# Optimization experiments

Hardware: AMD Instinct MI355X
Metric: run time of the kernel (lower is better)

The kernel has to match this reference:

```python
import jax, jax.numpy as jnp
import numpy as np

B, T, HW, ENC, DEC, ATT, EMB, V = 32, 128, 14, 2048, 512, 512, 512, 10000
P = HW * HW  # num_pixels = 196


def setup_inputs() -> dict:
    key = jax.random.key(0)
    ks = jax.random.split(key, 24)
    s = 0.02
    inp = {
        'bimgs': jax.random.normal(ks[0], (B, HW, HW, ENC), dtype=jnp.float32),
        'bx': jax.random.randint(ks[1], (B, T), 0, V),
        # torch code assumes lengths sorted DESCENDING
        'bxlen': jnp.sort(jax.random.randint(ks[2], (B,), 1, T + 1))[::-1],
        'emb_W': jax.random.normal(ks[3], (V, EMB)) * s,
        'enc_att_W': jax.random.normal(ks[4], (ATT, ENC)) * s,
        'enc_att_b': jnp.zeros((ATT,)),
        'dec_att_W': jax.random.normal(ks[5], (ATT, DEC)) * s,
        'dec_att_b': jnp.zeros((ATT,)),
        'full_att_W': jax.random.normal(ks[6], (1, ATT)) * s,
        'full_att_b': jnp.zeros((1,)),
        'init_h_W': jax.random.normal(ks[7], (DEC, ENC)) * s,
        'init_h_b': jnp.zeros((DEC,)),
        'init_c_W': jax.random.normal(ks[8], (DEC, ENC)) * s,
        'init_c_b': jnp.zeros((DEC,)),
        'f_beta_W': jax.random.normal(ks[9], (ENC, DEC)) * s,
        'f_beta_b': jnp.zeros((ENC,)),
        'W_ih': jax.random.normal(ks[10], (4 * DEC, EMB + ENC)) * s,
        'b_ih': jnp.zeros((4 * DEC,)),
        'W_hh': jax.random.normal(ks[11], (4 * DEC, DEC)) * s,
        'b_hh': jnp.zeros((4 * DEC,)),
        'fc_W': jax.random.normal(ks[12], (V, DEC)) * s,
        'fc_b': jnp.zeros((V,)),
    }
    return inp


def reference(bimgs, bx, bxlen, emb_W, enc_att_W, enc_att_b, dec_att_W, dec_att_b,
              full_att_W, full_att_b, init_h_W, init_h_b, init_c_W, init_c_b,
              f_beta_W, f_beta_b, W_ih, b_ih, W_hh, b_hh, fc_W, fc_b):
    b = bimgs.shape[0]
    imgs = bimgs.reshape(b, -1, bimgs.shape[-1])          # [B,P,enc]
    t_len = bx.shape[-1]
    embeds = emb_W[bx]                                     # [B,T,E]
    mean_img = imgs.mean(axis=1)                           # [B,enc]
    h0 = mean_img @ init_h_W.T + init_h_b                  # [B,dec]
    c0 = mean_img @ init_c_W.T + init_c_b
    # encoder attention projection is time-invariant -> hoist out of the loop
    att1 = imgs @ enc_att_W.T + enc_att_b                  # [B,P,A]
    active_ts = jnp.arange(t_len)[:, None] < bxlen[None, :]  # [T,B]
    emb_ts = embeds.transpose(1, 0, 2)                     # [T,B,E]

    def step(carry, xs):
        h, c = carry
        emb_t, active = xs
        att2 = h @ dec_att_W.T + dec_att_b                 # [B,A]
        e = jax.nn.relu(att1 + att2[:, None, :]) @ full_att_W[0] + full_att_b[0]  # [B,P]
        alpha = jax.nn.softmax(e, axis=1)
        awe = jnp.einsum('bpe,bp->be', imgs, alpha)        # [B,enc]
        gate = jax.nn.sigmoid(h @ f_beta_W.T + f_beta_b)
        x = jnp.concatenate([emb_t, gate * awe], axis=1)   # [B,E+enc]
        # PyTorch LSTMCell: gate order i, f, g, o
        gates = x @ W_ih.T + b_ih + h @ W_hh.T + b_hh
        i_, f_, g_, o_ = jnp.split(gates, 4, axis=1)
        i_ = jax.nn.sigmoid(i_); f_ = jax.nn.sigmoid(f_); o_ = jax.nn.sigmoid(o_)
        g_ = jnp.tanh(g_)
        c_new = f_ * c + i_ * g_
        h_new = o_ * jnp.tanh(c_new)
        preds = h_new @ fc_W.T + fc_b                      # dropout = identity (eval)
        m = active[:, None]
        h2 = jnp.where(m, h_new, h)
        c2 = jnp.where(m, c_new, c)
        return (h2, c2), (jnp.where(m, preds, 0.0), jnp.where(m, alpha, 0.0))

    _, (preds_ts, alphas_ts) = jax.lax.scan(step, (h0, c0), (emb_ts, active_ts))
    predictions = preds_ts.transpose(1, 0, 2)              # [B,T,V]
    alphas = alphas_ts.transpose(1, 0, 2)                  # [B,T,P]
    return predictions, alphas
```

## Files before the change

### kernel.cpp

```cpp
#include <hip/hip_runtime.h>
#include <hip/hip_bf16.h>

#define BB 32
#define TT 128
#define PP 196
#define ENC 2048
#define DEC 512
#define ATT 512
#define EMB 512
#define VV 10000
#define G4 2048
#define KX 2560

typedef unsigned short u16;
typedef unsigned int u32;
typedef __attribute__((ext_vector_type(8))) short short8;
typedef __attribute__((ext_vector_type(4))) float f32x4;

__device__ __forceinline__ float bf2f(u16 u) { return __uint_as_float(((u32)u) << 16); }
__device__ __forceinline__ u16 f2bf(float f) {
  u32 x = __float_as_uint(f);
  u32 r = (x + 0x7fffu + ((x >> 16) & 1u)) >> 16;
  return (u16)r;
}
__device__ __forceinline__ void unpack8(uint4 v, float* f) {
  f[0] = __uint_as_float(v.x << 16); f[1] = __uint_as_float(v.x & 0xffff0000u);
  f[2] = __uint_as_float(v.y << 16); f[3] = __uint_as_float(v.y & 0xffff0000u);
  f[4] = __uint_as_float(v.z << 16); f[5] = __uint_as_float(v.z & 0xffff0000u);
  f[6] = __uint_as_float(v.w << 16); f[7] = __uint_as_float(v.w & 0xffff0000u);
}
__device__ __forceinline__ void load8(const float* __restrict__ p, float* f) {
  float4 a = ((const float4*)p)[0];
  float4 b = ((const float4*)p)[1];
  f[0] = a.x; f[1] = a.y; f[2] = a.z; f[3] = a.w;
  f[4] = b.x; f[5] = b.y; f[6] = b.z; f[7] = b.w;
}
__device__ __forceinline__ float sigf(float x) { return 1.0f / (1.0f + __expf(-x)); }
__device__ __forceinline__ short8 ld_frag(const u16* __restrict__ p) {
  union { uint4 u; short8 s; } cv;
  cv.u = *(const uint4*)p;
  return cv.s;
}

__global__ __launch_bounds__(256) void k_cvt(const float* __restrict__ src, u16* __restrict__ dst, int n) {
  int i0 = (blockIdx.x * 256 + threadIdx.x) * 8;
  if (i0 >= n) return;
  float f[8]; load8(src + i0, f);
  u16 o[8];
#pragma unroll
  for (int u = 0; u < 8; u++) o[u] = f2bf(f[u]);
  *(uint4*)(dst + i0) = *(const uint4*)o;
}

__global__ __launch_bounds__(256) void k_mean(const u16* __restrict__ imgs_bf, u16* __restrict__ mean_bf) {
  int b = blockIdx.x >> 2, chunk = blockIdx.x & 3;
  int ch0 = chunk * 512 + threadIdx.x * 2;
  const u32* base = (const u32*)(imgs_bf + (size_t)b * PP * ENC + ch0);
  float a0 = 0.f, a1 = 0.f;
#pragma unroll 4
  for (int p = 0; p < PP; p++) {
    u32 u = base[(size_t)p * (ENC / 2)];
    a0 += __uint_as_float(u << 16);
    a1 += __uint_as_float(u & 0xffff0000u);
  }
  const float inv = 1.0f / PP;
  u16 o[2] = { f2bf(a0 * inv), f2bf(a1 * inv) };
  *(u32*)(mean_bf + b * ENC + ch0) = *(const u32*)o;
}

__global__ __launch_bounds__(64) void k_init2(const u16* __restrict__ W2_bf,
    const float* __restrict__ ihb, const float* __restrict__ icb,
    const u16* __restrict__ mean_bf, u16* __restrict__ h_bf, float* __restrict__ c) {
  int lane = threadIdx.x;
  int j0 = blockIdx.x * 16;
  int m = lane & 15, quad = lane >> 4;
  const u16* arow = W2_bf + (size_t)(j0 + m) * ENC + quad * 8;
  const u16* xb0 = mean_bf + (size_t)m * ENC + quad * 8;
  const u16* xb1 = mean_bf + (size_t)(16 + m) * ENC + quad * 8;
  f32x4 acc0 = {0.f,0.f,0.f,0.f}, acc1 = {0.f,0.f,0.f,0.f};
  for (int k = 0; k < ENC; k += 32) {
    short8 a = ld_frag(arow + k);
    short8 x0 = ld_frag(xb0 + k);
    short8 x1 = ld_frag(xb1 + k);
    acc0 = __builtin_amdgcn_mfma_f32_16x16x32_bf16(a, x0, acc0, 0, 0, 0);
    acc1 = __builtin_amdgcn_mfma_f32_16x16x32_bf16(a, x1, acc1, 0, 0, 0);
  }
  int jj = j0 + quad * 4;
  int b0 = m, b1 = 16 + m;
#pragma unroll
  for (int r = 0; r < 4; r++) {
    int j = jj + r;
    if (j < 512) {
      float bia = ihb[j];
      h_bf[b0 * DEC + j] = f2bf(acc0[r] + bia);
      h_bf[b1 * DEC + j] = f2bf(acc1[r] + bia);
    } else {
      int g = j - 512;
      float bia = icb[g];
      c[b0 * DEC + g] = acc0[r] + bia;
      c[b1 * DEC + g] = acc1[r] + bia;
    }
  }
}

__global__ __launch_bounds__(256) void k_att1(const u16* __restrict__ imgs_bf,
    const u16* __restrict__ encW_bf, const float* __restrict__ encb, u16* __restrict__ att1) {
  int tid = threadIdx.x;
  int wave = tid >> 6, lane = tid & 63;
  int m0 = blockIdx.x * 32;
  int lm = lane & 15, quad = lane >> 4;
  const u16* b0p = imgs_bf + (size_t)(m0 + lm) * ENC + quad * 8;
  const u16* b1p = imgs_bf + (size_t)(m0 + 16 + lm) * ENC + quad * 8;
  const u16* arow = encW_bf + (size_t)(wave * 128 + lm) * ENC + quad * 8;
  f32x4 acc[8][2];
#pragma unroll
  for (int i = 0; i < 8; i++) { acc[i][0] = (f32x4){0.f,0.f,0.f,0.f}; acc[i][1] = (f32x4){0.f,0.f,0.f,0.f}; }
  for (int k = 0; k < ENC; k += 32) {
    short8 B0 = ld_frag(b0p + k);
    short8 B1 = ld_frag(b1p + k);
#pragma unroll
    for (int i = 0; i < 8; i++) {
      short8 A = ld_frag(arow + (size_t)i * 16 * ENC + k);
      acc[i][0] = __builtin_amdgcn_mfma_f32_16x16x32_bf16(A, B0, acc[i][0], 0, 0, 0);
      acc[i][1] = __builtin_amdgcn_mfma_f32_16x16x32_bf16(A, B1, acc[i][1], 0, 0, 0);
    }
  }
#pragma unroll
  for (int i = 0; i < 8; i++) {
    int jb = wave * 128 + i * 16 + quad * 4;
#pragma unroll
    for (int r = 0; r < 4; r++) {
      int j = jb + r;
      float bia = encb[j];
      att1[(size_t)(m0 + lm) * ATT + j]      = f2bf(acc[i][0][r] + bia);
      att1[(size_t)(m0 + 16 + lm) * ATT + j] = f2bf(acc[i][1][r] + bia);
    }
  }
}

__global__ __launch_bounds__(64) void k_stage1(int t,
    const int* __restrict__ bx, const int* __restrict__ bxlen,
    const u16* __restrict__ W3, const float* __restrict__ decb,
    const float* __restrict__ fbb, const float* __restrict__ bhh,
    const u16* __restrict__ h_bf,
    float* __restrict__ att2, float* __restrict__ gate, float* __restrict__ hWhh,
    const u16* __restrict__ fcW_bf, const float* __restrict__ fcb, float* __restrict__ preds,
    const float* __restrict__ embW, u16* __restrict__ x_bf) {
  int bid = blockIdx.x;
  int lane = threadIdx.x;
  if (bid < 288) {
    if (t >= TT) return;
    int j0 = bid * 16;
    int m = lane & 15, quad = lane >> 4;
    const u16* arow = W3 + (size_t)(j0 + m) * DEC + quad * 8;
    const u16* xb0 = h_bf + (size_t)m * DEC + quad * 8;
    const u16* xb1 = h_bf + (size_t)(16 + m) * DEC + quad * 8;
    f32x4 acc0 = {0.f,0.f,0.f,0.f}, acc1 = {0.f,0.f,0.f,0.f};
    for (int k = 0; k < DEC; k += 32) {
      short8 a = ld_frag(arow + k);
      short8 x0 = ld_frag(xb0 + k);
      short8 x1 = ld_frag(xb1 + k);
      acc0 = __builtin_amdgcn_mfma_f32_16x16x32_bf16(a, x0, acc0, 0, 0, 0);
      acc1 = __builtin_amdgcn_mfma_f32_16x16x32_bf16(a, x1, acc1, 0, 0, 0);
    }
    int jj = j0 + quad * 4;
    int b0 = m, b1 = 16 + m;
#pragma unroll
    for (int r = 0; r < 4; r++) {
      int j = jj + r;
      float v0 = acc0[r], v1 = acc1[r];
      if (j0 < ATT) {
        float bia = decb[j];
        att2[b0 * ATT + j] = v0 + bia;
        att2[b1 * ATT + j] = v1 + bia;
      } else if (j0 < ATT + ENC) {
        int g = j - ATT;
        float bia = fbb[g];
        gate[b0 * ENC + g] = sigf(v0 + bia);
        gate[b1 * ENC + g] = sigf(v1 + bia);
      } else {
        int g = j - ATT - ENC;
        float bia = bhh[g];
        hWhh[b0 * G4 + g] = v0 + bia;
        hWhh[b1 * G4 + g] = v1 + bia;
      }
    }
  } else if (bid < 913) {
    if (t == 0) return;
    int tfc = t - 1;
    int j0 = (bid - 288) * 16;
    int m = lane & 15, quad = lane >> 4;
    const u16* arow = fcW_bf + (size_t)(j0 + m) * DEC + quad * 8;
    const u16* xb0 = h_bf + (size_t)m * DEC + quad * 8;
    const u16* xb1 = h_bf + (size_t)(16 + m) * DEC + quad * 8;
    f32x4 acc0 = {0.f,0.f,0.f,0.f}, acc1 = {0.f,0.f,0.f,0.f};
    for (int k = 0; k < DEC; k += 32) {
      short8 a = ld_frag(arow + k);
      short8 x0 = ld_frag(xb0 + k);
      short8 x1 = ld_frag(xb1 + k);
      acc0 = __builtin_amdgcn_mfma_f32_16x16x32_bf16(a, x0, acc0, 0, 0, 0);
      acc1 = __builtin_amdgcn_mfma_f32_16x16x32_bf16(a, x1, acc1, 0, 0, 0);
    }
    int jj = j0 + quad * 4;
    int b0 = m, b1 = 16 + m;
    bool act0 = (tfc < bxlen[b0]);
    bool act1 = (tfc < bxlen[b1]);
#pragma unroll
    for (int r = 0; r < 4; r++) {
      int j = jj + r;
      float bia = fcb[j];
      preds[((size_t)b0 * TT + tfc) * VV + j] = act0 ? (acc0[r] + bia) : 0.f;
      preds[((size_t)b1 * TT + tfc) * VV + j] = act1 ? (acc1[r] + bia) : 0.f;
    }
  } else {
    if (t >= TT) return;
    int flat = (bid - 913) * 64 + lane;
    int b = flat >> 5;
    int ch0 = (flat & 31) * 16;
    int tok = bx[b * TT + t];
    const float* e = embW + (size_t)tok * EMB + ch0;
    u16 o[16];
#pragma unroll
    for (int u = 0; u < 16; u++) o[u] = f2bf(e[u]);
    *(uint4*)(x_bf + (size_t)b * KX + ch0)     = *(const uint4*)o;
    *(uint4*)(x_bf + (size_t)b * KX + ch0 + 8) = *(const uint4*)(o + 8);
  }
}

__global__ __launch_bounds__(256) void k_att(int t, const int* __restrict__ bxlen,
    const u16* __restrict__ att1, const float* __restrict__ att2,
    const float* __restrict__ faW, const float* __restrict__ fab,
    float* __restrict__ alpha_ws, float* __restrict__ out_alphas) {
  int b = blockIdx.x;
  int tid = threadIdx.x;
  if (t >= bxlen[b]) {
    if (tid < PP) out_alphas[((size_t)b * TT + t) * PP + tid] = 0.f;
    return;
  }
  __shared__ float a2[ATT];
  __shared__ float w_s[ATT];
  __shared__ float redw[4], redw2[4];
  for (int i = tid; i < ATT; i += 256) { a2[i] = att2[b * ATT + i]; w_s[i] = faW[i]; }
  __syncthreads();
  float e = -1e30f;
  if (tid < PP) {
    const uint4* ar = (const uint4*)(att1 + (size_t)(b * PP + tid) * ATT);
    float acc = 0.f;
    for (int k = 0; k < ATT; k += 8) {
      float af[8]; unpack8(ar[k >> 3], af);
#pragma unroll
      for (int u = 0; u < 8; u++) {
        float v = af[u] + a2[k + u];
        acc += fmaxf(v, 0.f) * w_s[k + u];
      }
    }
    e = acc + fab[0];
  }
  int lane = tid & 63, wid = tid >> 6;
  float wmax = e;
#pragma unroll
  for (int off = 32; off; off >>= 1) wmax = fmaxf(wmax, __shfl_xor(wmax, off));
  if (lane == 0) redw[wid] = wmax;
  __syncthreads();
  float mx = fmaxf(fmaxf(redw[0], redw[1]), fmaxf(redw[2], redw[3]));
  float ex = (tid < PP) ? __expf(e - mx) : 0.f;
  float wsum = ex;
#pragma unroll
  for (int off = 32; off; off >>= 1) wsum += __shfl_xor(wsum, off);
  if (lane == 0) redw2[wid] = wsum;
  __syncthreads();
  float inv = 1.0f / (redw2[0] + redw2[1] + redw2[2] + redw2[3]);
  if (tid < PP) {
    float al = ex * inv;
    alpha_ws[b * PP + tid] = al;
    out_alphas[((size_t)b * TT + t) * PP + tid] = al;
  }
}

__global__ __launch_bounds__(256) void k_awe(int t, const int* __restrict__ bxlen,
    const u16* __restrict__ imgs_bf, const float* __restrict__ alpha_ws,
    const float* __restrict__ gate, u16* __restrict__ x_bf) {
  int b = blockIdx.x >> 2, chunk = blockIdx.x & 3;
  if (t >= bxlen[b]) return;
  __shared__ float al[PP];
  int tid = threadIdx.x;
  if (tid < PP) al[tid] = alpha_ws[b * PP + tid];
  __syncthreads();
  int ch0 = chunk * 512 + tid * 2;
  const u32* base = (const u32*)(imgs_bf + (size_t)b * PP * ENC + ch0);
  float acc0 = 0.f, acc1 = 0.f;
#pragma unroll 4
  for (int p = 0; p < PP; p++) {
    u32 u = base[(size_t)p * (ENC / 2)];
    float a = al[p];
    acc0 += a * __uint_as_float(u << 16);
    acc1 += a * __uint_as_float(u & 0xffff0000u);
  }
  float2 g = *(const float2*)(gate + b * ENC + ch0);
  u16 o[2] = { f2bf(g.x * acc0), f2bf(g.y * acc1) };
  *(u32*)(x_bf + (size_t)b * KX + EMB + ch0) = *(const u32*)o;
}

__global__ __launch_bounds__(64) void k_gates(const u16* __restrict__ Wih_bf,
    const u16* __restrict__ x_bf, float* __restrict__ gates_p) {
  int lane = threadIdx.x;
  int j0 = blockIdx.x * 16;
  int kc = blockIdx.y * 640;
  int m = lane & 15, quad = lane >> 4;
  const u16* arow = Wih_bf + (size_t)(j0 + m) * KX + kc + quad * 8;
  const u16* xb0 = x_bf + (size_t)m * KX + kc + quad * 8;
  const u16* xb1 = x_bf + (size_t)(16 + m) * KX + kc + quad * 8;
  f32x4 acc0 = {0.f,0.f,0.f,0.f}, acc1 = {0.f,0.f,0.f,0.f};
  for (int k = 0; k < 640; k += 32) {
    short8 a = ld_frag(arow + k);
    short8 x0 = ld_frag(xb0 + k);
    short8 x1 = ld_frag(xb1 + k);
    acc0 = __builtin_amdgcn_mfma_f32_16x16x32_bf16(a, x0, acc0, 0, 0, 0);
    acc1 = __builtin_amdgcn_mfma_f32_16x16x32_bf16(a, x1, acc1, 0, 0, 0);
  }
  float* gp = gates_p + (size_t)blockIdx.y * BB * G4;
  int jj = j0 + quad * 4;
  int b0 = m, b1 = 16 + m;
#pragma unroll
  for (int r = 0; r < 4; r++) {
    int j = jj + r;
    gp[b0 * G4 + j] = acc0[r];
    gp[b1 * G4 + j] = acc1[r];
  }
}

__global__ __launch_bounds__(256) void k_lstm(int t, const int* __restrict__ bxlen,
    const float* __restrict__ gates_p, const float* __restrict__ bih,
    const float* __restrict__ hWhh,
    u16* __restrict__ h_bf, float* __restrict__ c) {
  int idx = blockIdx.x * 256 + threadIdx.x;
  int b = idx >> 9, d = idx & 511;
  if (t >= bxlen[b]) return;
  float pre[4];
#pragma unroll
  for (int g = 0; g < 4; g++) {
    int j = g * 512 + d;
    float s = bih[j] + hWhh[b * G4 + j];
#pragma unroll
    for (int cc = 0; cc < 4; cc++) s += gates_p[(size_t)cc * BB * G4 + b * G4 + j];
    pre[g] = s;
  }
  float i_ = sigf(pre[0]);
  float f_ = sigf(pre[1]);
  float g_ = tanhf(pre[2]);
  float o_ = sigf(pre[3]);
  float cn = f_ * c[b * DEC + d] + i_ * g_;
  float hn = o_ * tanhf(cn);
  c[b * DEC + d] = cn;
  h_bf[b * DEC + d] = f2bf(hn);
}

extern "C" void kernel_launch(void* const* d_in, const int* in_sizes, int n_in,
                              void* d_out, int out_size, void* d_ws, size_t ws_size,
                              hipStream_t stream) {
  const float* imgs = (const float*)d_in[0];
  const int* bx     = (const int*)d_in[1];
  const int* bxlen  = (const int*)d_in[2];
  const float* embW = (const float*)d_in[3];
  const float* encW = (const float*)d_in[4];
  const float* encb = (const float*)d_in[5];
  const float* decW = (const float*)d_in[6];
  const float* decb = (const float*)d_in[7];
  const float* faW  = (const float*)d_in[8];
  const float* fab  = (const float*)d_in[9];
  const float* ihW  = (const float*)d_in[10];
  const float* ihb  = (const float*)d_in[11];
  const float* icW  = (const float*)d_in[12];
  const float* icb  = (const float*)d_in[13];
  const float* fbW  = (const float*)d_in[14];
  const float* fbb  = (const float*)d_in[15];
  const float* Wih  = (const float*)d_in[16];
  const float* bih  = (const float*)d_in[17];
  const float* Whh  = (const float*)d_in[18];
  const float* bhh  = (const float*)d_in[19];
  const float* fcW  = (const float*)d_in[20];
  const float* fcb  = (const float*)d_in[21];

  float* out_preds  = (float*)d_out;
  float* out_alphas = out_preds + (size_t)BB * TT * VV;

  char* wsb = (char*)d_ws;
  size_t off = 0;
  u16* imgs_bf = (u16*)(wsb + off); off += (size_t)BB * PP * ENC * 2;
  u16* W3_bf   = (u16*)(wsb + off); off += (size_t)4608 * DEC * 2;
  u16* Wih_bf  = (u16*)(wsb + off); off += (size_t)G4 * KX * 2;
  u16* fcW_bf  = (u16*)(wsb + off); off += (size_t)VV * DEC * 2;
  u16* encW_bf = (u16*)(wsb + off); off += (size_t)ATT * ENC * 2;
  u16* att1    = (u16*)(wsb + off);
  u16* W2_bf   = att1;
  u16* mean_bf = att1 + (size_t)1024 * ENC;
  off += (size_t)BB * PP * ATT * 2;
  u16* x_bf    = (u16*)(wsb + off); off += (size_t)BB * KX * 2;
  u16* h_bf    = (u16*)(wsb + off); off += (size_t)BB * DEC * 2;
  float* c      = (float*)(wsb + off); off += (size_t)BB * DEC * 4;
  float* att2   = (float*)(wsb + off); off += (size_t)BB * ATT * 4;
  float* gate   = (float*)(wsb + off); off += (size_t)BB * ENC * 4;
  float* hWhh   = (float*)(wsb + off); off += (size_t)BB * G4 * 4;
  float* gates_p = (float*)(wsb + off); off += (size_t)4 * BB * G4 * 4;
  float* alpha  = (float*)(wsb + off); off += (size_t)BB * PP * 4;

  k_cvt<<<(BB * PP * ENC) / 2048, 256, 0, stream>>>(imgs, imgs_bf, BB * PP * ENC);
  k_cvt<<<(DEC * DEC) / 2048, 256, 0, stream>>>(decW, W3_bf, DEC * DEC);
  k_cvt<<<(ENC * DEC) / 2048, 256, 0, stream>>>(fbW, W3_bf + (size_t)DEC * DEC, ENC * DEC);
  k_cvt<<<(G4 * DEC) / 2048, 256, 0, stream>>>(Whh, W3_bf + (size_t)(DEC + ENC) * DEC, G4 * DEC);
  k_cvt<<<(G4 * KX) / 2048, 256, 0, stream>>>(Wih, Wih_bf, G4 * KX);
  k_cvt<<<(VV * DEC) / 2048, 256, 0, stream>>>(fcW, fcW_bf, VV * DEC);
  k_cvt<<<(ATT * ENC) / 2048, 256, 0, stream>>>(encW, encW_bf, ATT * ENC);
  k_cvt<<<(DEC * ENC) / 2048, 256, 0, stream>>>(ihW, W2_bf, DEC * ENC);
  k_cvt<<<(DEC * ENC) / 2048, 256, 0, stream>>>(icW, W2_bf + (size_t)DEC * ENC, DEC * ENC);

  k_mean<<<BB * 4, 256, 0, stream>>>(imgs_bf, mean_bf);
  k_init2<<<64, 64, 0, stream>>>(W2_bf, ihb, icb, mean_bf, h_bf, c);
  k_att1<<<(BB * PP) / 32, 256, 0, stream>>>(imgs_bf, encW_bf, encb, att1);

  for (int t = 0; t < TT; t++) {
    k_stage1<<<929, 64, 0, stream>>>(t, bx, bxlen, W3_bf, decb, fbb, bhh, h_bf,
                                     att2, gate, hWhh, fcW_bf, fcb, out_preds, embW, x_bf);
    k_att<<<BB, 256, 0, stream>>>(t, bxlen, att1, att2, faW, fab, alpha, out_alphas);
    k_awe<<<BB * 4, 256, 0, stream>>>(t, bxlen, imgs_bf, alpha, gate, x_bf);
    k_gates<<<dim3(G4 / 16, 4), 64, 0, stream>>>(Wih_bf, x_bf, gates_p);
    k_lstm<<<(BB * DEC) / 256, 256, 0, stream>>>(t, bxlen, gates_p, bih, hWhh, h_bf, c);
  }
  k_stage1<<<929, 64, 0, stream>>>(TT, bx, bxlen, W3_bf, decb, fbb, bhh, h_bf,
                                   att2, gate, hWhh, fcW_bf, fcb, out_preds, embW, x_bf);
}
```

Measured before the change: 6.786 ms.

## Fuse attention with weighted encoding and gate GEMM with LSTM cell

Merges the attention-score/softmax kernel with the attention-weighted-encoding kernel in a single 1024-thread block per batch row, keeping alpha in shared memory. It also merges the input-gate GEMM with the LSTM cell update: each block computes all four gate slices for 16 hidden units over the full K dimension, then applies the cell update from shared memory. This cuts per-step launches from five to three and removes the global round trips for alpha and the split-K partial gates. The cost is less parallelism: the gate GEMM drops from 512 split-K waves to 128 waves, each running the full K loop serially.

New measurement: 9.066 ms. 33.6% more time.

```diff
diff --git a/kernel.cpp b/kernel.cpp
--- a/kernel.cpp
+++ b/kernel.cpp
@@ -227,10 +227,11 @@
   }
 }
 
-__global__ __launch_bounds__(256) void k_att(int t, const int* __restrict__ bxlen,
+__global__ __launch_bounds__(1024) void k_attawe(int t, const int* __restrict__ bxlen,
     const u16* __restrict__ att1, const float* __restrict__ att2,
     const float* __restrict__ faW, const float* __restrict__ fab,
-    float* __restrict__ alpha_ws, float* __restrict__ out_alphas) {
+    const u16* __restrict__ imgs_bf, const float* __restrict__ gate,
+    float* __restrict__ out_alphas, u16* __restrict__ x_bf) {
   int b = blockIdx.x;
   int tid = threadIdx.x;
   if (t >= bxlen[b]) {
@@ -239,60 +240,58 @@
   }
   __shared__ float a2[ATT];
   __shared__ float w_s[ATT];
-  __shared__ float redw[4], redw2[4];
-  for (int i = tid; i < ATT; i += 256) { a2[i] = att2[b * ATT + i]; w_s[i] = faW[i]; }
-  __syncthreads();
-  float e = -1e30f;
-  if (tid < PP) {
-    const uint4* ar = (const uint4*)(att1 + (size_t)(b * PP + tid) * ATT);
+  __shared__ float alph[PP];
+  __shared__ float red1[16], red2[16];
+  if (tid < ATT) a2[tid] = att2[b * ATT + tid];
+  else w_s[tid - ATT] = faW[tid - ATT];
+  __syncthreads();
+  int p = tid >> 2, sub = tid & 3;
+  if (p < PP) {
+    const uint4* ar = (const uint4*)(att1 + (size_t)(b * PP + p) * ATT + sub * 128);
+    int kb = sub * 128;
     float acc = 0.f;
-    for (int k = 0; k < ATT; k += 8) {
+#pragma unroll
+    for (int k = 0; k < 128; k += 8) {
       float af[8]; unpack8(ar[k >> 3], af);
 #pragma unroll
       for (int u = 0; u < 8; u++) {
-        float v = af[u] + a2[k + u];
-        acc += fmaxf(v, 0.f) * w_s[k + u];
+        float v = af[u] + a2[kb + k + u];
+        acc += fmaxf(v, 0.f) * w_s[kb + k + u];
       }
     }
-    e = acc + fab[0];
-  }
+    acc += __shfl_xor(acc, 1);
+    acc += __shfl_xor(acc, 2);
+    if (sub == 0) alph[p] = acc + fab[0];
+  }
+  __syncthreads();
+  float v = (tid < PP) ? alph[tid] : -1e30f;
   int lane = tid & 63, wid = tid >> 6;
-  float wmax = e;
+  float wmax = v;
 #pragma unroll
   for (int off = 32; off; off >>= 1) wmax = fmaxf(wmax, __shfl_xor(wmax, off));
-  if (lane == 0) redw[wid] = wmax;
-  __syncthreads();
-  float mx = fmaxf(fmaxf(redw[0], redw[1]), fmaxf(redw[2], redw[3]));
-  float ex = (tid < PP) ? __expf(e - mx) : 0.f;
+  if (lane == 0) red1[wid] = wmax;
+  __syncthreads();
+  float mx = fmaxf(fmaxf(red1[0], red1[1]), fmaxf(red1[2], red1[3]));
+  float ex = (tid < PP) ? __expf(v - mx) : 0.f;
   float wsum = ex;
 #pragma unroll
   for (int off = 32; off; off >>= 1) wsum += __shfl_xor(wsum, off);
-  if (lane == 0) redw2[wid] = wsum;
-  __syncthreads();
-  float inv = 1.0f / (redw2[0] + redw2[1] + redw2[2] + redw2[3]);
+  if (lane == 0) red2[wid] = wsum;
+  __syncthreads();
+  float inv = 1.0f / (red2[0] + red2[1] + red2[2] + red2[3]);
   if (tid < PP) {
     float al = ex * inv;
-    alpha_ws[b * PP + tid] = al;
+    alph[tid] = al;
     out_alphas[((size_t)b * TT + t) * PP + tid] = al;
   }
-}
-
-__global__ __launch_bounds__(256) void k_awe(int t, const int* __restrict__ bxlen,
-    const u16* __restrict__ imgs_bf, const float* __restrict__ alpha_ws,
-    const float* __restrict__ gate, u16* __restrict__ x_bf) {
-  int b = blockIdx.x >> 2, chunk = blockIdx.x & 3;
-  if (t >= bxlen[b]) return;
-  __shared__ float al[PP];
-  int tid = threadIdx.x;
-  if (tid < PP) al[tid] = alpha_ws[b * PP + tid];
-  __syncthreads();
-  int ch0 = chunk * 512 + tid * 2;
+  __syncthreads();
+  int ch0 = tid * 2;
   const u32* base = (const u32*)(imgs_bf + (size_t)b * PP * ENC + ch0);
   float acc0 = 0.f, acc1 = 0.f;
 #pragma unroll 4
-  for (int p = 0; p < PP; p++) {
-    u32 u = base[(size_t)p * (ENC / 2)];
-    float a = al[p];
+  for (int pp = 0; pp < PP; pp++) {
+    u32 u = base[(size_t)pp * (ENC / 2)];
+    float a = alph[pp];
     acc0 += a * __uint_as_float(u << 16);
     acc1 += a * __uint_as_float(u & 0xffff0000u);
   }
@@ -301,58 +300,49 @@
   *(u32*)(x_bf + (size_t)b * KX + EMB + ch0) = *(const u32*)o;
 }
 
-__global__ __launch_bounds__(64) void k_gates(const u16* __restrict__ Wih_bf,
-    const u16* __restrict__ x_bf, float* __restrict__ gates_p) {
-  int lane = threadIdx.x;
-  int j0 = blockIdx.x * 16;
-  int kc = blockIdx.y * 640;
+__global__ __launch_bounds__(256) void k_gateslstm(int t, const int* __restrict__ bxlen,
+    const u16* __restrict__ Wih_bf, const float* __restrict__ bih,
+    const u16* __restrict__ x_bf, const float* __restrict__ hWhh,
+    u16* __restrict__ h_bf, float* __restrict__ c) {
+  __shared__ float pre_s[4][16][33];
+  int tid = threadIdx.x;
+  int wave = tid >> 6, lane = tid & 63;
+  int g = blockIdx.x;
   int m = lane & 15, quad = lane >> 4;
-  const u16* arow = Wih_bf + (size_t)(j0 + m) * KX + kc + quad * 8;
-  const u16* xb0 = x_bf + (size_t)m * KX + kc + quad * 8;
-  const u16* xb1 = x_bf + (size_t)(16 + m) * KX + kc + quad * 8;
+  int jbase = wave * 512 + g * 16;
+  const u16* arow = Wih_bf + (size_t)(jbase + m) * KX + quad * 8;
+  const u16* xb0 = x_bf + (size_t)m * KX + quad * 8;
+  const u16* xb1 = x_bf + (size_t)(16 + m) * KX + quad * 8;
   f32x4 acc0 = {0.f,0.f,0.f,0.f}, acc1 = {0.f,0.f,0.f,0.f};
-  for (int k = 0; k < 640; k += 32) {
+#pragma unroll 4
+  for (int k = 0; k < KX; k += 32) {
     short8 a = ld_frag(arow + k);
     short8 x0 = ld_frag(xb0 + k);
     short8 x1 = ld_frag(xb1 + k);
     acc0 = __builtin_amdgcn_mfma_f32_16x16x32_bf16(a, x0, acc0, 0, 0, 0);
     acc1 = __builtin_amdgcn_mfma_f32_16x16x32_bf16(a, x1, acc1, 0, 0, 0);
   }
-  float* gp = gates_p + (size_t)blockIdx.y * BB * G4;
-  int jj = j0 + quad * 4;
-  int b0 = m, b1 = 16 + m;
+  int dd = quad * 4;
 #pragma unroll
   for (int r = 0; r < 4; r++) {
-    int j = jj + r;
-    gp[b0 * G4 + j] = acc0[r];
-    gp[b1 * G4 + j] = acc1[r];
-  }
-}
-
-__global__ __launch_bounds__(256) void k_lstm(int t, const int* __restrict__ bxlen,
-    const float* __restrict__ gates_p, const float* __restrict__ bih,
-    const float* __restrict__ hWhh,
-    u16* __restrict__ h_bf, float* __restrict__ c) {
-  int idx = blockIdx.x * 256 + threadIdx.x;
-  int b = idx >> 9, d = idx & 511;
-  if (t >= bxlen[b]) return;
-  float pre[4];
-#pragma unroll
-  for (int g = 0; g < 4; g++) {
-    int j = g * 512 + d;
-    float s = bih[j] + hWhh[b * G4 + j];
-#pragma unroll
-    for (int cc = 0; cc < 4; cc++) s += gates_p[(size_t)cc * BB * G4 + b * G4 + j];
-    pre[g] = s;
-  }
-  float i_ = sigf(pre[0]);
-  float f_ = sigf(pre[1]);
-  float g_ = tanhf(pre[2]);
-  float o_ = sigf(pre[3]);
-  float cn = f_ * c[b * DEC + d] + i_ * g_;
-  float hn = o_ * tanhf(cn);
-  c[b * DEC + d] = cn;
-  h_bf[b * DEC + d] = f2bf(hn);
+    pre_s[wave][dd + r][m]      = acc0[r];
+    pre_s[wave][dd + r][16 + m] = acc1[r];
+  }
+  __syncthreads();
+  for (int i = tid; i < 512; i += 256) {
+    int d_idx = i >> 5, b = i & 31;
+    if (t >= bxlen[b]) continue;
+    int d = g * 16 + d_idx;
+    float p0 = pre_s[0][d_idx][b] + bih[d]        + hWhh[b * G4 + d];
+    float p1 = pre_s[1][d_idx][b] + bih[512 + d]  + hWhh[b * G4 + 512 + d];
+    float p2 = pre_s[2][d_idx][b] + bih[1024 + d] + hWhh[b * G4 + 1024 + d];
+    float p3 = pre_s[3][d_idx][b] + bih[1536 + d] + hWhh[b * G4 + 1536 + d];
+    float i_ = sigf(p0), f_ = sigf(p1), g_ = tanhf(p2), o_ = sigf(p3);
+    float cn = f_ * c[b * DEC + d] + i_ * g_;
+    float hn = o_ * tanhf(cn);
+    c[b * DEC + d] = cn;
+    h_bf[b * DEC + d] = f2bf(hn);
+  }
 }
 
 extern "C" void kernel_launch(void* const* d_in, const int* in_sizes, int n_in,
@@ -401,8 +391,6 @@
   float* att2   = (float*)(wsb + off); off += (size_t)BB * ATT * 4;
   float* gate   = (float*)(wsb + off); off += (size_t)BB * ENC * 4;
   float* hWhh   = (float*)(wsb + off); off += (size_t)BB * G4 * 4;
-  float* gates_p = (float*)(wsb + off); off += (size_t)4 * BB * G4 * 4;
-  float* alpha  = (float*)(wsb + off); off += (size_t)BB * PP * 4;
 
   k_cvt<<<(BB * PP * ENC) / 2048, 256, 0, stream>>>(imgs, imgs_bf, BB * PP * ENC);
   k_cvt<<<(DEC * DEC) / 2048, 256, 0, stream>>>(decW, W3_bf, DEC * DEC);
@@ -421,10 +409,9 @@
   for (int t = 0; t < TT; t++) {
     k_stage1<<<929, 64, 0, stream>>>(t, bx, bxlen, W3_bf, decb, fbb, bhh, h_bf,
                                      att2, gate, hWhh, fcW_bf, fcb, out_preds, embW, x_bf);
-    k_att<<<BB, 256, 0, stream>>>(t, bxlen, att1, att2, faW, fab, alpha, out_alphas);
-    k_awe<<<BB * 4, 256, 0, stream>>>(t, bxlen, imgs_bf, alpha, gate, x_bf);
-    k_gates<<<dim3(G4 / 16, 4), 64, 0, stream>>>(Wih_bf, x_bf, gates_p);
-    k_lstm<<<(BB * DEC) / 256, 256, 0, stream>>>(t, bxlen, gates_p, bih, hWhh, h_bf, c);
+    k_attawe<<<BB, 1024, 0, stream>>>(t, bxlen, att1, att2, faW, fab, imgs_bf, gate,
+                                      out_alphas, x_bf);
+    k_gateslstm<<<BB, 256, 0, stream>>>(t, bxlen, Wih_bf, bih, x_bf, hWhh, h_bf, c);
   }
   k_stage1<<<929, 64, 0, stream>>>(TT, bx, bxlen, W3_bf, decb, fbb, bhh, h_bf,
                                    att2, gate, hWhh, fcW_bf, fcb, out_preds, embW, x_bf);
```

## Hoist output projection out of recurrence into one batched GEMM over all steps

Applied to the files above, without the earlier changes.

The vocabulary projection no longer runs inside every time step. Each step's hidden state is now stored in a history buffer, and after the loop one large MFMA GEMM computes all predictions with a weight tile shared across 32 rows. Embedding lookups for every step are also gathered and converted to bf16 once up front, and the input-gate GEMM is split into five K-chunks to match the separate embedding and attention-context buffers. This removes re-streaming the 10k×512 fc weight on each step and shortens the serial per-step chain, at the cost of extra workspace and one more partial-sum read in the LSTM kernel.

Measured after the change: 6.265 ms. 1.08x faster.

```diff
diff --git a/kernel.cpp b/kernel.cpp
--- a/kernel.cpp
+++ b/kernel.cpp
@@ -9,6 +9,7 @@
 #define ATT 512
 #define EMB 512
 #define VV 10000
+#define VVP 10240
 #define G4 2048
 #define KX 2560
 
@@ -50,6 +51,20 @@
 #pragma unroll
   for (int u = 0; u < 8; u++) o[u] = f2bf(f[u]);
   *(uint4*)(dst + i0) = *(const uint4*)o;
+}
+
+__global__ __launch_bounds__(256) void k_emball(const int* __restrict__ bx,
+    const float* __restrict__ embW, u16* __restrict__ xemb) {
+  int flat = blockIdx.x * 256 + threadIdx.x;
+  int row = flat >> 6;
+  int c8 = (flat & 63) * 8;
+  int tok = bx[row];
+  const float* e = embW + (size_t)tok * EMB + c8;
+  float f[8]; load8(e, f);
+  u16 o[8];
+#pragma unroll
+  for (int u = 0; u < 8; u++) o[u] = f2bf(f[u]);
+  *(uint4*)(xemb + (size_t)row * EMB + c8) = *(const uint4*)o;
 }
 
 __global__ __launch_bounds__(256) void k_mean(const u16* __restrict__ imgs_bf, u16* __restrict__ mean_bf) {
@@ -138,92 +153,45 @@
   }
 }
 
-__global__ __launch_bounds__(64) void k_stage1(int t,
-    const int* __restrict__ bx, const int* __restrict__ bxlen,
-    const u16* __restrict__ W3, const float* __restrict__ decb,
-    const float* __restrict__ fbb, const float* __restrict__ bhh,
+__global__ __launch_bounds__(64) void k_step1(const u16* __restrict__ W3,
+    const float* __restrict__ decb, const float* __restrict__ fbb, const float* __restrict__ bhh,
     const u16* __restrict__ h_bf,
-    float* __restrict__ att2, float* __restrict__ gate, float* __restrict__ hWhh,
-    const u16* __restrict__ fcW_bf, const float* __restrict__ fcb, float* __restrict__ preds,
-    const float* __restrict__ embW, u16* __restrict__ x_bf) {
-  int bid = blockIdx.x;
+    float* __restrict__ att2, float* __restrict__ gate, float* __restrict__ hWhh) {
   int lane = threadIdx.x;
-  if (bid < 288) {
-    if (t >= TT) return;
-    int j0 = bid * 16;
-    int m = lane & 15, quad = lane >> 4;
-    const u16* arow = W3 + (size_t)(j0 + m) * DEC + quad * 8;
-    const u16* xb0 = h_bf + (size_t)m * DEC + quad * 8;
-    const u16* xb1 = h_bf + (size_t)(16 + m) * DEC + quad * 8;
-    f32x4 acc0 = {0.f,0.f,0.f,0.f}, acc1 = {0.f,0.f,0.f,0.f};
-    for (int k = 0; k < DEC; k += 32) {
-      short8 a = ld_frag(arow + k);
-      short8 x0 = ld_frag(xb0 + k);
-      short8 x1 = ld_frag(xb1 + k);
-      acc0 = __builtin_amdgcn_mfma_f32_16x16x32_bf16(a, x0, acc0, 0, 0, 0);
-      acc1 = __builtin_amdgcn_mfma_f32_16x16x32_bf16(a, x1, acc1, 0, 0, 0);
-    }
-    int jj = j0 + quad * 4;
-    int b0 = m, b1 = 16 + m;
-#pragma unroll
-    for (int r = 0; r < 4; r++) {
-      int j = jj + r;
-      float v0 = acc0[r], v1 = acc1[r];
-      if (j0 < ATT) {
-        float bia = decb[j];
-        att2[b0 * ATT + j] = v0 + bia;
-        att2[b1 * ATT + j] = v1 + bia;
-      } else if (j0 < ATT + ENC) {
-        int g = j - ATT;
-        float bia = fbb[g];
-        gate[b0 * ENC + g] = sigf(v0 + bia);
-        gate[b1 * ENC + g] = sigf(v1 + bia);
-      } else {
-        int g = j - ATT - ENC;
-        float bia = bhh[g];
-        hWhh[b0 * G4 + g] = v0 + bia;
-        hWhh[b1 * G4 + g] = v1 + bia;
-      }
-    }
-  } else if (bid < 913) {
-    if (t == 0) return;
-    int tfc = t - 1;
-    int j0 = (bid - 288) * 16;
-    int m = lane & 15, quad = lane >> 4;
-    const u16* arow = fcW_bf + (size_t)(j0 + m) * DEC + quad * 8;
-    const u16* xb0 = h_bf + (size_t)m * DEC + quad * 8;
-    const u16* xb1 = h_bf + (size_t)(16 + m) * DEC + quad * 8;
-    f32x4 acc0 = {0.f,0.f,0.f,0.f}, acc1 = {0.f,0.f,0.f,0.f};
-    for (int k = 0; k < DEC; k += 32) {
-      short8 a = ld_frag(arow + k);
-      short8 x0 = ld_frag(xb0 + k);
-      short8 x1 = ld_frag(xb1 + k);
-      acc0 = __builtin_amdgcn_mfma_f32_16x16x32_bf16(a, x0, acc0, 0, 0, 0);
-      acc1 = __builtin_amdgcn_mfma_f32_16x16x32_bf16(a, x1, acc1, 0, 0, 0);
-    }
-    int jj = j0 + quad * 4;
-    int b0 = m, b1 = 16 + m;
-    bool act0 = (tfc < bxlen[b0]);
-    bool act1 = (tfc < bxlen[b1]);
-#pragma unroll
-    for (int r = 0; r < 4; r++) {
-      int j = jj + r;
-      float bia = fcb[j];
-      preds[((size_t)b0 * TT + tfc) * VV + j] = act0 ? (acc0[r] + bia) : 0.f;
-      preds[((size_t)b1 * TT + tfc) * VV + j] = act1 ? (acc1[r] + bia) : 0.f;
-    }
-  } else {
-    if (t >= TT) return;
-    int flat = (bid - 913) * 64 + lane;
-    int b = flat >> 5;
-    int ch0 = (flat & 31) * 16;
-    int tok = bx[b * TT + t];
-    const float* e = embW + (size_t)tok * EMB + ch0;
-    u16 o[16];
-#pragma unroll
-    for (int u = 0; u < 16; u++) o[u] = f2bf(e[u]);
-    *(uint4*)(x_bf + (size_t)b * KX + ch0)     = *(const uint4*)o;
-    *(uint4*)(x_bf + (size_t)b * KX + ch0 + 8) = *(const uint4*)(o + 8);
+  int j0 = blockIdx.x * 16;
+  int m = lane & 15, quad = lane >> 4;
+  const u16* arow = W3 + (size_t)(j0 + m) * DEC + quad * 8;
+  const u16* xb0 = h_bf + (size_t)m * DEC + quad * 8;
+  const u16* xb1 = h_bf + (size_t)(16 + m) * DEC + quad * 8;
+  f32x4 acc0 = {0.f,0.f,0.f,0.f}, acc1 = {0.f,0.f,0.f,0.f};
+  for (int k = 0; k < DEC; k += 32) {
+    short8 a = ld_frag(arow + k);
+    short8 x0 = ld_frag(xb0 + k);
+    short8 x1 = ld_frag(xb1 + k);
+    acc0 = __builtin_amdgcn_mfma_f32_16x16x32_bf16(a, x0, acc0, 0, 0, 0);
+    acc1 = __builtin_amdgcn_mfma_f32_16x16x32_bf16(a, x1, acc1, 0, 0, 0);
+  }
+  int jj = j0 + quad * 4;
+  int b0 = m, b1 = 16 + m;
+#pragma unroll
+  for (int r = 0; r < 4; r++) {
+    int j = jj + r;
+    float v0 = acc0[r], v1 = acc1[r];
+    if (j0 < ATT) {
+      float bia = decb[j];
+      att2[b0 * ATT + j] = v0 + bia;
+      att2[b1 * ATT + j] = v1 + bia;
+    } else if (j0 < ATT + ENC) {
+      int g = j - ATT;
+      float bia = fbb[g];
+      gate[b0 * ENC + g] = sigf(v0 + bia);
+      gate[b1 * ENC + g] = sigf(v1 + bia);
+    } else {
+      int g = j - ATT - ENC;
+      float bia = bhh[g];
+      hWhh[b0 * G4 + g] = v0 + bia;
+      hWhh[b1 * G4 + g] = v1 + bia;
+    }
   }
 }
 
@@ -279,7 +247,7 @@
 
 __global__ __launch_bounds__(256) void k_awe(int t, const int* __restrict__ bxlen,
     const u16* __restrict__ imgs_bf, const float* __restrict__ alpha_ws,
-    const float* __restrict__ gate, u16* __restrict__ x_bf) {
+    const float* __restrict__ gate, u16* __restrict__ x_awe) {
   int b = blockIdx.x >> 2, chunk = blockIdx.x & 3;
   if (t >= bxlen[b]) return;
   __shared__ float al[PP];
@@ -298,27 +266,36 @@
   }
   float2 g = *(const float2*)(gate + b * ENC + ch0);
   u16 o[2] = { f2bf(g.x * acc0), f2bf(g.y * acc1) };
-  *(u32*)(x_bf + (size_t)b * KX + EMB + ch0) = *(const u32*)o;
-}
-
-__global__ __launch_bounds__(64) void k_gates(const u16* __restrict__ Wih_bf,
-    const u16* __restrict__ x_bf, float* __restrict__ gates_p) {
+  *(u32*)(x_awe + (size_t)b * ENC + ch0) = *(const u32*)o;
+}
+
+__global__ __launch_bounds__(64) void k_gates(int t, const u16* __restrict__ Wih_bf,
+    const u16* __restrict__ xemb, const u16* __restrict__ x_awe,
+    float* __restrict__ gates_p) {
   int lane = threadIdx.x;
   int j0 = blockIdx.x * 16;
-  int kc = blockIdx.y * 640;
+  int y = blockIdx.y;
+  int kofs = y * 512;
   int m = lane & 15, quad = lane >> 4;
-  const u16* arow = Wih_bf + (size_t)(j0 + m) * KX + kc + quad * 8;
-  const u16* xb0 = x_bf + (size_t)m * KX + kc + quad * 8;
-  const u16* xb1 = x_bf + (size_t)(16 + m) * KX + kc + quad * 8;
+  const u16* arow = Wih_bf + (size_t)(j0 + m) * KX + kofs + quad * 8;
+  const u16 *b0p, *b1p;
+  if (y == 0) {
+    b0p = xemb + ((size_t)m * TT + t) * EMB + quad * 8;
+    b1p = xemb + ((size_t)(16 + m) * TT + t) * EMB + quad * 8;
+  } else {
+    int ao = kofs - 512;
+    b0p = x_awe + (size_t)m * ENC + ao + quad * 8;
+    b1p = x_awe + (size_t)(16 + m) * ENC + ao + quad * 8;
+  }
   f32x4 acc0 = {0.f,0.f,0.f,0.f}, acc1 = {0.f,0.f,0.f,0.f};
-  for (int k = 0; k < 640; k += 32) {
+  for (int k = 0; k < 512; k += 32) {
     short8 a = ld_frag(arow + k);
-    short8 x0 = ld_frag(xb0 + k);
-    short8 x1 = ld_frag(xb1 + k);
+    short8 x0 = ld_frag(b0p + k);
+    short8 x1 = ld_frag(b1p + k);
     acc0 = __builtin_amdgcn_mfma_f32_16x16x32_bf16(a, x0, acc0, 0, 0, 0);
     acc1 = __builtin_amdgcn_mfma_f32_16x16x32_bf16(a, x1, acc1, 0, 0, 0);
   }
-  float* gp = gates_p + (size_t)blockIdx.y * BB * G4;
+  float* gp = gates_p + (size_t)y * BB * G4;
   int jj = j0 + quad * 4;
   int b0 = m, b1 = 16 + m;
 #pragma unroll
@@ -332,7 +309,7 @@
 __global__ __launch_bounds__(256) void k_lstm(int t, const int* __restrict__ bxlen,
     const float* __restrict__ gates_p, const float* __restrict__ bih,
     const float* __restrict__ hWhh,
-    u16* __restrict__ h_bf, float* __restrict__ c) {
+    u16* __restrict__ h_bf, float* __restrict__ c, u16* __restrict__ h_hist) {
   int idx = blockIdx.x * 256 + threadIdx.x;
   int b = idx >> 9, d = idx & 511;
   if (t >= bxlen[b]) return;
@@ -342,7 +319,7 @@
     int j = g * 512 + d;
     float s = bih[j] + hWhh[b * G4 + j];
 #pragma unroll
-    for (int cc = 0; cc < 4; cc++) s += gates_p[(size_t)cc * BB * G4 + b * G4 + j];
+    for (int cc = 0; cc < 5; cc++) s += gates_p[(size_t)cc * BB * G4 + b * G4 + j];
     pre[g] = s;
   }
   float i_ = sigf(pre[0]);
@@ -352,7 +329,51 @@
   float cn = f_ * c[b * DEC + d] + i_ * g_;
   float hn = o_ * tanhf(cn);
   c[b * DEC + d] = cn;
-  h_bf[b * DEC + d] = f2bf(hn);
+  u16 hb = f2bf(hn);
+  h_bf[b * DEC + d] = hb;
+  h_hist[((size_t)b * TT + t) * DEC + d] = hb;
+}
+
+__global__ __launch_bounds__(256) void k_fcall(const int* __restrict__ bxlen,
+    const u16* __restrict__ fcW_bf, const float* __restrict__ fcb,
+    const u16* __restrict__ h_hist, float* __restrict__ preds) {
+  int tid = threadIdx.x;
+  int wave = tid >> 6, lane = tid & 63;
+  int m0 = blockIdx.x * 32;
+  int jbase = blockIdx.y * 512 + wave * 128;
+  int lm = lane & 15, quad = lane >> 4;
+  const u16* b0p = h_hist + (size_t)(m0 + lm) * DEC + quad * 8;
+  const u16* b1p = h_hist + (size_t)(m0 + 16 + lm) * DEC + quad * 8;
+  const u16* arow = fcW_bf + (size_t)(jbase + lm) * DEC + quad * 8;
+  f32x4 acc[8][2];
+#pragma unroll
+  for (int i = 0; i < 8; i++) { acc[i][0] = (f32x4){0.f,0.f,0.f,0.f}; acc[i][1] = (f32x4){0.f,0.f,0.f,0.f}; }
+  for (int k = 0; k < DEC; k += 32) {
+    short8 B0 = ld_frag(b0p + k);
+    short8 B1 = ld_frag(b1p + k);
+#pragma unroll
+    for (int i = 0; i < 8; i++) {
+      short8 A = ld_frag(arow + (size_t)i * 16 * DEC + k);
+      acc[i][0] = __builtin_amdgcn_mfma_f32_16x16x32_bf16(A, B0, acc[i][0], 0, 0, 0);
+      acc[i][1] = __builtin_amdgcn_mfma_f32_16x16x32_bf16(A, B1, acc[i][1], 0, 0, 0);
+    }
+  }
+  int row0 = m0 + lm, row1 = m0 + 16 + lm;
+  bool act0 = ((row0 & 127) < bxlen[row0 >> 7]);
+  bool act1 = ((row1 & 127) < bxlen[row1 >> 7]);
+#pragma unroll
+  for (int i = 0; i < 8; i++) {
+    int jb = jbase + i * 16 + quad * 4;
+#pragma unroll
+    for (int r = 0; r < 4; r++) {
+      int j = jb + r;
+      if (j < VV) {
+        float bia = fcb[j];
+        preds[(size_t)row0 * VV + j] = act0 ? (acc[i][0][r] + bia) : 0.f;
+        preds[(size_t)row1 * VV + j] = act1 ? (acc[i][1][r] + bia) : 0.f;
+      }
+    }
+  }
 }
 
 extern "C" void kernel_launch(void* const* d_in, const int* in_sizes, int n_in,
@@ -389,19 +410,21 @@
   u16* imgs_bf = (u16*)(wsb + off); off += (size_t)BB * PP * ENC * 2;
   u16* W3_bf   = (u16*)(wsb + off); off += (size_t)4608 * DEC * 2;
   u16* Wih_bf  = (u16*)(wsb + off); off += (size_t)G4 * KX * 2;
-  u16* fcW_bf  = (u16*)(wsb + off); off += (size_t)VV * DEC * 2;
+  u16* fcW_bf  = (u16*)(wsb + off); off += (size_t)VVP * DEC * 2;
   u16* encW_bf = (u16*)(wsb + off); off += (size_t)ATT * ENC * 2;
   u16* att1    = (u16*)(wsb + off);
   u16* W2_bf   = att1;
   u16* mean_bf = att1 + (size_t)1024 * ENC;
   off += (size_t)BB * PP * ATT * 2;
-  u16* x_bf    = (u16*)(wsb + off); off += (size_t)BB * KX * 2;
+  u16* xemb    = (u16*)(wsb + off); off += (size_t)BB * TT * EMB * 2;
+  u16* h_hist  = (u16*)(wsb + off); off += (size_t)BB * TT * DEC * 2;
+  u16* x_awe   = (u16*)(wsb + off); off += (size_t)BB * ENC * 2;
   u16* h_bf    = (u16*)(wsb + off); off += (size_t)BB * DEC * 2;
   float* c      = (float*)(wsb + off); off += (size_t)BB * DEC * 4;
   float* att2   = (float*)(wsb + off); off += (size_t)BB * ATT * 4;
   float* gate   = (float*)(wsb + off); off += (size_t)BB * ENC * 4;
   float* hWhh   = (float*)(wsb + off); off += (size_t)BB * G4 * 4;
-  float* gates_p = (float*)(wsb + off); off += (size_t)4 * BB * G4 * 4;
+  float* gates_p = (float*)(wsb + off); off += (size_t)5 * BB * G4 * 4;
   float* alpha  = (float*)(wsb + off); off += (size_t)BB * PP * 4;
 
   k_cvt<<<(BB * PP * ENC) / 2048, 256, 0, stream>>>(imgs, imgs_bf, BB * PP * ENC);
@@ -413,19 +436,18 @@
   k_cvt<<<(ATT * ENC) / 2048, 256, 0, stream>>>(encW, encW_bf, ATT * ENC);
   k_cvt<<<(DEC * ENC) / 2048, 256, 0, stream>>>(ihW, W2_bf, DEC * ENC);
   k_cvt<<<(DEC * ENC) / 2048, 256, 0, stream>>>(icW, W2_bf + (size_t)DEC * ENC, DEC * ENC);
+  k_emball<<<(BB * TT * EMB / 8) / 256, 256, 0, stream>>>(bx, embW, xemb);
 
   k_mean<<<BB * 4, 256, 0, stream>>>(imgs_bf, mean_bf);
   k_init2<<<64, 64, 0, stream>>>(W2_bf, ihb, icb, mean_bf, h_bf, c);
   k_att1<<<(BB * PP) / 32, 256, 0, stream>>>(imgs_bf, encW_bf, encb, att1);
 
   for (int t = 0; t < TT; t++) {
-    k_stage1<<<929, 64, 0, stream>>>(t, bx, bxlen, W3_bf, decb, fbb, bhh, h_bf,
-                                     att2, gate, hWhh, fcW_bf, fcb, out_preds, embW, x_bf);
+    k_step1<<<4608 / 16, 64, 0, stream>>>(W3_bf, decb, fbb, bhh, h_bf, att2, gate, hWhh);
     k_att<<<BB, 256, 0, stream>>>(t, bxlen, att1, att2, faW, fab, alpha, out_alphas);
-    k_awe<<<BB * 4, 256, 0, stream>>>(t, bxlen, imgs_bf, alpha, gate, x_bf);
-    k_gates<<<dim3(G4 / 16, 4), 64, 0, stream>>>(Wih_bf, x_bf, gates_p);
-    k_lstm<<<(BB * DEC) / 256, 256, 0, stream>>>(t, bxlen, gates_p, bih, hWhh, h_bf, c);
-  }
-  k_stage1<<<929, 64, 0, stream>>>(TT, bx, bxlen, W3_bf, decb, fbb, bhh, h_bf,
-                                   att2, gate, hWhh, fcW_bf, fcb, out_preds, embW, x_bf);
-}
+    k_awe<<<BB * 4, 256, 0, stream>>>(t, bxlen, imgs_bf, alpha, gate, x_awe);
+    k_gates<<<dim3(G4 / 16, 5), 64, 0, stream>>>(t, Wih_bf, xemb, x_awe, gates_p);
+    k_lstm<<<(BB * DEC) / 256, 256, 0, stream>>>(t, bxlen, gates_p, bih, hWhh, h_bf, c, h_hist);
+  }
+  k_fcall<<<dim3((BB * TT) / 32, 20), 256, 0, stream>>>(bxlen, fcW_bf, fcb, h_hist, out_preds);
+}
```
